# Kernel optimization log

Hardware: AMD Instinct MI355X
Metric: run time of the kernel (lower is better)

## Reference

```python
import jax, jax.numpy as jnp
import numpy as np

D_MODEL, D_STATE, D_INNER, DT_RANK, D_CONV, K = 768, 16, 1536, 48, 3, 2
B_SZ, L_SEQ = 2, 2048

def setup_inputs() -> dict:
    key = jax.random.key(0)
    ks = jax.random.split(key, 10)
    s = lambda k, shp, sc=0.02: jax.random.normal(k, shp, dtype=jnp.float32) * sc
    return {
        "x": jax.random.normal(ks[0], (B_SZ, L_SEQ, D_MODEL), dtype=jnp.float32),
        "in_proj_w": s(ks[1], (2 * D_INNER, D_MODEL)),
        "conv_w": s(ks[2], (D_INNER, 1, D_CONV), 0.3),
        "conv_b": s(ks[3], (D_INNER,), 0.1),
        "x_proj_w": s(ks[4], (K, DT_RANK + 2 * D_STATE, D_INNER)),
        "dt_proj_w": s(ks[5], (K, D_INNER, DT_RANK), 0.1),
        "dt_proj_b": s(ks[6], (K, D_INNER), 0.1),
        "A_logs": s(ks[7], (K * D_INNER, D_STATE), 0.5),
        "Ds": jnp.ones((K * D_INNER,), dtype=jnp.float32),
        "out_proj_w": s(ks[8], (D_MODEL, D_INNER)),
    }

def _selective_scan(u, delta, A, Bp, Cp, Dk):
    # u, delta: [B, L, D]; A: [D, N]; Bp, Cp: [B, L, N]; Dk: [D]
    def step(h, inp):
        d_t, u_t, b_t, c_t = inp  # [B,D], [B,D], [B,N], [B,N]
        dA = jnp.exp(d_t[..., None] * A)  # [B,D,N]
        h = h * dA + (d_t * u_t)[..., None] * b_t[:, None, :]
        y_t = jnp.einsum('bdn,bn->bd', h, c_t)
        return h, y_t
    h0 = jnp.zeros((u.shape[0], u.shape[2], A.shape[1]), dtype=u.dtype)
    xs = (jnp.swapaxes(delta, 0, 1), jnp.swapaxes(u, 0, 1),
          jnp.swapaxes(Bp, 0, 1), jnp.swapaxes(Cp, 0, 1))
    _, ys = jax.lax.scan(step, h0, xs)  # ys: [L, B, D]
    return jnp.swapaxes(ys, 0, 1) + u * Dk  # [B, L, D]

def _direction(u_k, xw_k, dtw_k, dtb_k, Alog_k, D_k):
    x_dbl = jnp.einsum('bld,rd->blr', u_k, xw_k)
    dt_in, Bp, Cp = jnp.split(x_dbl, [DT_RANK, DT_RANK + D_STATE], axis=-1)
    delta = jax.nn.softplus(jnp.einsum('blr,dr->bld', dt_in, dtw_k) + dtb_k)
    A = -jnp.exp(Alog_k)
    return _selective_scan(u_k, delta, A, Bp, Cp, D_k)

def reference(x, in_proj_w, conv_w, conv_b, x_proj_w, dt_proj_w, dt_proj_b, A_logs, Ds, out_proj_w):
    xz = x @ in_proj_w.T                       # [B, L, 2*Din]
    x_conv, z = jnp.split(xz, 2, axis=-1)
    xc = jnp.swapaxes(x_conv, 1, 2)            # [B, Din, L]
    pad = (D_CONV - 1) // 2
    xc = jax.lax.conv_general_dilated(
        xc, conv_w, window_strides=(1,), padding=[(pad, pad)],
        feature_group_count=D_INNER, dimension_numbers=('NCH', 'OIH', 'NCH'))
    xc = xc + conv_b[None, :, None]
    u = jnp.swapaxes(jax.nn.silu(xc), 1, 2)    # [B, L, Din]

    u_dirs = jnp.stack([u, jnp.flip(u, axis=1)])          # [K, B, L, Din]
    A_logs_k = A_logs.reshape(K, D_INNER, D_STATE)
    Ds_k = Ds.reshape(K, D_INNER)
    y_dirs = jax.vmap(_direction)(u_dirs, x_proj_w, dt_proj_w, dt_proj_b, A_logs_k, Ds_k)
    y_scanned = y_dirs[0] + jnp.flip(y_dirs[1], axis=1)
    y_gated = y_scanned * z
    return y_gated @ out_proj_w.T
```

## Files before the change

### kernel.cpp

```cpp
#include <hip/hip_runtime.h>
#include <math.h>

#define D_MODEL 768
#define D_STATE 16
#define D_INNER 1536
#define DT_RANK 48
#define B_SZ    2
#define L_SEQ   2048
#define CH      64
#define NCH     (L_SEQ / CH)
#define NDG     24
#define MTOT    (B_SZ * L_SEQ)
#define LOG2E   1.4426950408889634f
#define LN2     0.6931471805599453f

typedef __bf16 bf16x8 __attribute__((ext_vector_type(8)));
typedef float f32x4 __attribute__((ext_vector_type(4)));
typedef ushort ushort8_t __attribute__((ext_vector_type(8)));

__device__ __forceinline__ float ex2(float x) {
  return __builtin_amdgcn_exp2f(x);
}

__device__ __forceinline__ ushort f2bf(float f) {
  unsigned int u = __float_as_uint(f);
  unsigned int r = (u + 0x7fff + ((u >> 16) & 1)) >> 16;
  return (ushort)r;
}
__device__ __forceinline__ float bf2f(ushort u) {
  return __uint_as_float(((unsigned int)u) << 16);
}

__device__ __forceinline__ void gload_lds16(const ushort* g, ushort* l) {
  __builtin_amdgcn_global_load_lds(
      (__attribute__((address_space(1))) void*)(void*)(g),
      (__attribute__((address_space(3))) void*)(void*)(l), 16, 0, 0);
}

__device__ __forceinline__ float softplus_fast(float x) {
  return (x > 20.f) ? x : LN2 * __log2f(1.f + ex2(x * LOG2E));
}

template <int BM, int BN, int ACT, int OBF, int DTOUT>
__device__ __forceinline__ void gemm_body(
    const ushort* __restrict__ A, int lda, const ushort* __restrict__ B,
    int ldb, const float* __restrict__ bias, void* __restrict__ Cp, int ldc,
    int Nreal, int K, int bxi, int byi, ushort* __restrict__ dtin) {
  __shared__ ushort As[2][BM][32];
  __shared__ ushort Bs[2][BN][32];
  constexpr int WM = BM / 2, WN = BN / 2;
  constexpr int FM = WM / 16, FN = WN / 16;
  const int tid = threadIdx.x;
  const int lane = tid & 63;
  const int w = tid >> 6;
  const int wr = w >> 1, wc = w & 1;
  const int bm = byi * BM, bn = bxi * BN;
  const int lrow = lane >> 2;
  const int lchunk = lane & 3;
  const int fr = lane & 15;
  const int k8 = (lane >> 4) * 8;

  f32x4 acc[FM][FN] = {};

  auto stage = [&](int buf, int k0) {
    if constexpr (BM >= 64) {
#pragma unroll
      for (int g = 0; g < BM / 64; ++g) {
        const int rb = w * (BM / 4) + g * 16;
        gload_lds16(A + (size_t)(bm + rb + lrow) * lda + k0 + lchunk * 8,
                    &As[buf][rb][0]);
      }
    } else {
      if (w < 2)
        gload_lds16(A + (size_t)(bm + w * 16 + lrow) * lda + k0 + lchunk * 8,
                    &As[buf][w * 16][0]);
    }
#pragma unroll
    for (int g = 0; g < BN / 64; ++g) {
      const int rb = w * (BN / 4) + g * 16;
      gload_lds16(B + (size_t)(bn + rb + lrow) * ldb + k0 + lchunk * 8,
                  &Bs[buf][rb][0]);
    }
  };

  stage(0, 0);
  __syncthreads();
  int cur = 0;
  for (int k0 = 0; k0 < K; k0 += 32) {
    if (k0 + 32 < K) stage(cur ^ 1, k0 + 32);
    bf16x8 af[FM], bfr[FN];
#pragma unroll
    for (int m = 0; m < FM; ++m)
      af[m] =
          *reinterpret_cast<const bf16x8*>(&As[cur][wr * WM + m * 16 + fr][k8]);
#pragma unroll
    for (int n = 0; n < FN; ++n)
      bfr[n] =
          *reinterpret_cast<const bf16x8*>(&Bs[cur][wc * WN + n * 16 + fr][k8]);
#pragma unroll
    for (int m = 0; m < FM; ++m)
#pragma unroll
      for (int n = 0; n < FN; ++n)
        acc[m][n] = __builtin_amdgcn_mfma_f32_16x16x32_bf16(af[m], bfr[n],
                                                            acc[m][n], 0, 0, 0);
    __syncthreads();
    cur ^= 1;
  }

  const int row4 = (lane >> 4) * 4;
#pragma unroll
  for (int m = 0; m < FM; ++m) {
#pragma unroll
    for (int n = 0; n < FN; ++n) {
      const int gn = bn + wc * WN + n * 16 + fr;
      const int gm0 = bm + wr * WM + m * 16 + row4;
#pragma unroll
      for (int j = 0; j < 4; ++j) {
        const float v = acc[m][n][j];
        const int gm = gm0 + j;
        if (DTOUT) {
          if (gn < 64)
            dtin[(size_t)gm * 64 + gn] = (gn < 48) ? f2bf(v) : (ushort)0;
          else if (gn >= 80 && gn < 144)
            dtin[(size_t)MTOT * 64 + (size_t)gm * 64 + (gn - 80)] =
                (gn < 128) ? f2bf(v) : (ushort)0;
        }
        if (gn < Nreal) {
          float vv = v + (bias ? bias[gn] : 0.f);
          if (ACT == 1) vv = softplus_fast(vv);
          if (OBF)
            ((ushort*)Cp)[(size_t)gm * ldc + gn] = f2bf(vv);
          else
            ((float*)Cp)[(size_t)gm * ldc + gn] = vv;
        }
      }
    }
  }
}

template <int BM, int BN, int ACT, int OBF, int DTOUT>
__global__ __launch_bounds__(256) void gemm_k(
    const ushort* __restrict__ A, int lda, const ushort* __restrict__ B,
    int ldb, const float* __restrict__ bias, void* __restrict__ Cp, int ldc,
    int Nreal, int K, ushort* __restrict__ dtin) {
  gemm_body<BM, BN, ACT, OBF, DTOUT>(A, lda, B, ldb, bias, Cp, ldc, Nreal, K,
                                     blockIdx.x, blockIdx.y, dtin);
}

__global__ __launch_bounds__(256) void gemm_dt_k(
    const ushort* __restrict__ dtin, const ushort* __restrict__ w_dt,
    const float* __restrict__ dtb, ushort* __restrict__ delta) {
  const int k = blockIdx.z;
  gemm_body<64, 128, 1, 1, 0>(
      dtin + (size_t)k * MTOT * 64, 64, w_dt + (size_t)k * D_INNER * 64, 64,
      dtb + k * D_INNER, delta + (size_t)k * MTOT * D_INNER, D_INNER, D_INNER,
      64, blockIdx.x, blockIdx.y, nullptr);
}

__global__ __launch_bounds__(256) void cvt_all_kernel(
    const float* __restrict__ x, const float* __restrict__ w_in,
    const float* __restrict__ w_out, const float* __restrict__ w_xp,
    const float* __restrict__ w_dt, ushort* __restrict__ x_bf,
    ushort* __restrict__ w_in_bf, ushort* __restrict__ w_out_bf,
    ushort* __restrict__ w_xp_bf, ushort* __restrict__ w_dt_bf) {
  const long N0 = 3145728, N1 = 2359296, N2 = 1179648, N3 = 393216, N4 = 196608;
  long i = ((long)blockIdx.x * 256 + threadIdx.x) * 4;
  if (i < N0) {
    const float4 v = *(const float4*)(x + i);
    ushort4 o = {f2bf(v.x), f2bf(v.y), f2bf(v.z), f2bf(v.w)};
    *(ushort4*)(x_bf + i) = o;
    return;
  }
  i -= N0;
  if (i < N1) {
    const float4 v = *(const float4*)(w_in + i);
    ushort4 o = {f2bf(v.x), f2bf(v.y), f2bf(v.z), f2bf(v.w)};
    *(ushort4*)(w_in_bf + i) = o;
    return;
  }
  i -= N1;
  if (i < N2) {
    const float4 v = *(const float4*)(w_out + i);
    ushort4 o = {f2bf(v.x), f2bf(v.y), f2bf(v.z), f2bf(v.w)};
    *(ushort4*)(w_out_bf + i) = o;
    return;
  }
  i -= N2;
  if (i < N3) {
    const long row = i / 1536;
    ushort4 o = {0, 0, 0, 0};
    if (row < 160) {
      const float4 v = *(const float4*)(w_xp + i);
      o.x = f2bf(v.x); o.y = f2bf(v.y); o.z = f2bf(v.z); o.w = f2bf(v.w);
    }
    *(ushort4*)(w_xp_bf + i) = o;
    return;
  }
  i -= N3;
  if (i < N4) {
    const int col = (int)(i & 63);
    const long row = i >> 6;
    ushort4 o = {0, 0, 0, 0};
    if (col < 48) {
      const float4 v = *(const float4*)(w_dt + row * 48 + col);
      o.x = f2bf(v.x); o.y = f2bf(v.y); o.z = f2bf(v.z); o.w = f2bf(v.w);
    }
    *(ushort4*)(w_dt_bf + i) = o;
  }
}

__global__ __launch_bounds__(256) void conv_silu_kernel(
    const ushort* __restrict__ xz, const float* __restrict__ cw,
    const float* __restrict__ cb, ushort* __restrict__ u_bf) {
  const int nd8 = D_INNER / 8;
  const int idx = blockIdx.x * 256 + threadIdx.x;
  const int d8 = idx % nd8;
  const int lg = (idx / nd8) % (L_SEQ / 8);
  const int b = idx / (nd8 * (L_SEQ / 8));
  const int d = d8 * 8;
  const int l0 = lg * 8;

  float w0[8], w1[8], w2[8], bs[8];
#pragma unroll
  for (int j = 0; j < 8; ++j) {
    w0[j] = cw[(d + j) * 3 + 0];
    w1[j] = cw[(d + j) * 3 + 1];
    w2[j] = cw[(d + j) * 3 + 2];
    bs[j] = cb[d + j];
  }
  const ushort* base = xz + ((size_t)b * L_SEQ) * 3072 + d;
  const ushort8_t zv = {0, 0, 0, 0, 0, 0, 0, 0};
  ushort8_t prev = (l0 > 0) ? *(const ushort8_t*)(base + (size_t)(l0 - 1) * 3072) : zv;
  ushort8_t curv = *(const ushort8_t*)(base + (size_t)l0 * 3072);
#pragma unroll
  for (int i = 0; i < 8; ++i) {
    const int l = l0 + i;
    const ushort8_t nxt =
        (l + 1 < L_SEQ) ? *(const ushort8_t*)(base + (size_t)(l + 1) * 3072) : zv;
    ushort8_t o;
#pragma unroll
    for (int j = 0; j < 8; ++j) {
      const float a = bs[j] + bf2f(prev[j]) * w0[j] + bf2f(curv[j]) * w1[j] +
                      bf2f(nxt[j]) * w2[j];
      o[j] = f2bf(a / (1.f + __expf(-a)));
    }
    *(ushort8_t*)(u_bf + ((size_t)b * L_SEQ + l) * D_INNER + d) = o;
    prev = curv;
    curv = nxt;
  }
}

__global__ __launch_bounds__(128) void scan_local_kernel(
    const ushort* __restrict__ u_bf, const float* __restrict__ xdbl,
    const ushort* __restrict__ delta_bf, const float* __restrict__ A_logs,
    const float* __restrict__ Ds, ushort* __restrict__ y,
    float* __restrict__ hfin, float* __restrict__ Tsum) {
  __shared__ ushort sdu[32][64];
  __shared__ ushort suu[32][64];
  __shared__ float sB[32][16], sC[32][16];
  const int tid = threadIdx.x;
  const int lane = tid & 63;
  const int w = tid >> 6;
  const int chW = lane >> 1;
  const int half = lane & 1;
  const int bid = blockIdx.x;
  const int ch = bid & (NCH - 1);
  const int rest = bid >> 5;
  const int dgB = rest % NDG;
  const int kb = rest / NDG;
  const int b = kb & 1;
  const int k = kb >> 1;
  const int d0 = dgB * 64;
  const int dl = w * 32 + chW;
  const int d = d0 + dl;
  const int row = k * D_INNER + d;

  float An[8];
  {
    const float4 a0 =
        *(const float4*)(A_logs + (size_t)row * D_STATE + half * 8);
    const float4 a1 =
        *(const float4*)(A_logs + (size_t)row * D_STATE + half * 8 + 4);
    An[0] = -__expf(a0.x) * LOG2E; An[1] = -__expf(a0.y) * LOG2E;
    An[2] = -__expf(a0.z) * LOG2E; An[3] = -__expf(a0.w) * LOG2E;
    An[4] = -__expf(a1.x) * LOG2E; An[5] = -__expf(a1.y) * LOG2E;
    An[6] = -__expf(a1.z) * LOG2E; An[7] = -__expf(a1.w) * LOG2E;
  }
  const float Dk = Ds[row];

  const ushort* uptr = u_bf + ((size_t)b * L_SEQ) * D_INNER;
  const ushort* dptr = delta_bf + ((size_t)(k * B_SZ + b) * L_SEQ) * D_INNER;
  const float* xptr = xdbl + ((size_t)b * L_SEQ) * 160 + k * 80;
  ushort* yptr = y + ((size_t)(k * B_SZ + b) * L_SEQ) * D_INNER;

  float h[8] = {};
  float S = 0.f;

  for (int sub = 0; sub < CH / 32; ++sub) {
    const int t0 = ch * CH + sub * 32;
    const int lbase = k ? (L_SEQ - 32 - t0) : t0;
    {
      const ushort* src = (w == 0) ? dptr : uptr;
      ushort* dst = (w == 0) ? &sdu[0][0] : &suu[0][0];
#pragma unroll
      for (int i = 0; i < 4; ++i) {
        const int rd = i * 8 + (lane >> 3);
        const int gr = k ? (31 - rd) : rd;
        const int seg = lane & 7;
        gload_lds16(src + (size_t)(lbase + gr) * D_INNER + d0 + seg * 8,
                    dst + i * 512);
      }
    }
    {
      const int r = lane >> 1;
      const int ridx = k ? (31 - r) : r;
      const int c8 = (lane & 1) * 8;
      const float* srcx =
          xptr + (size_t)(lbase + r) * 160 + DT_RANK + (w ? D_STATE : 0) + c8;
      float* dstx = (w == 0) ? &sB[ridx][c8] : &sC[ridx][c8];
      *(float4*)dstx = *(const float4*)srcx;
      *(float4*)(dstx + 4) = *(const float4*)(srcx + 4);
    }
    __syncthreads();
    for (int s = 0; s < 32; ++s) {
      const float dlt = bf2f(sdu[s][dl]);
      const float uu = bf2f(suu[s][dl]);
      S += dlt;
      const float du = dlt * uu;
      const float4 Bv0 = *(const float4*)&sB[s][half * 8];
      const float4 Bv1 = *(const float4*)&sB[s][half * 8 + 4];
      const float4 Cv0 = *(const float4*)&sC[s][half * 8];
      const float4 Cv1 = *(const float4*)&sC[s][half * 8 + 4];
      h[0] = h[0] * ex2(dlt * An[0]) + du * Bv0.x;
      h[1] = h[1] * ex2(dlt * An[1]) + du * Bv0.y;
      h[2] = h[2] * ex2(dlt * An[2]) + du * Bv0.z;
      h[3] = h[3] * ex2(dlt * An[3]) + du * Bv0.w;
      h[4] = h[4] * ex2(dlt * An[4]) + du * Bv1.x;
      h[5] = h[5] * ex2(dlt * An[5]) + du * Bv1.y;
      h[6] = h[6] * ex2(dlt * An[6]) + du * Bv1.z;
      h[7] = h[7] * ex2(dlt * An[7]) + du * Bv1.w;
      float yt = h[0] * Cv0.x + h[1] * Cv0.y + h[2] * Cv0.z + h[3] * Cv0.w +
                 h[4] * Cv1.x + h[5] * Cv1.y + h[6] * Cv1.z + h[7] * Cv1.w;
      yt += __shfl_xor(yt, 1);
      if (half == 0) {
        const int t = t0 + s;
        const int l = k ? (L_SEQ - 1 - t) : t;
        yptr[(size_t)l * D_INNER + d] = f2bf(yt + uu * Dk);
      }
    }
    __syncthreads();
  }

  const size_t cidxB = ((size_t)(k * B_SZ + b) * NCH + ch) * NDG + dgB;
  *(float4*)(hfin + cidxB * 1024 + dl * 16 + half * 8) =
      make_float4(h[0], h[1], h[2], h[3]);
  *(float4*)(hfin + cidxB * 1024 + dl * 16 + half * 8 + 4) =
      make_float4(h[4], h[5], h[6], h[7]);
  if (half == 0) Tsum[cidxB * 64 + dl] = S;
}

__global__ __launch_bounds__(256) void scan_stitch_kernel(
    const float* __restrict__ hfin, const float* __restrict__ Tsum,
    const float* __restrict__ A_logs, float* __restrict__ hin) {
  const int tid = threadIdx.x;
  const int dl = tid >> 2;
  const int nq = tid & 3;
  const int bid = blockIdx.x;
  const int dgB = bid % NDG;
  const int b = (bid / NDG) & 1;
  const int k = bid / (NDG * 2);
  const int row = k * D_INNER + dgB * 64 + dl;
  const float4 alv = *(const float4*)(A_logs + (size_t)row * D_STATE + nq * 4);
  const float An0 = -__expf(alv.x) * LOG2E, An1 = -__expf(alv.y) * LOG2E;
  const float An2 = -__expf(alv.z) * LOG2E, An3 = -__expf(alv.w) * LOG2E;
  float c0 = 0.f, c1 = 0.f, c2 = 0.f, c3 = 0.f;
  for (int ch = 0; ch < NCH; ++ch) {
    const size_t cidxB = ((size_t)(k * B_SZ + b) * NCH + ch) * NDG + dgB;
    const size_t off = cidxB * 1024 + dl * 16 + nq * 4;
    *(float4*)(hin + off) = make_float4(c0, c1, c2, c3);
    const float T = Tsum[cidxB * 64 + dl];
    const float4 hf = *(const float4*)(hfin + off);
    c0 = c0 * ex2(An0 * T) + hf.x;
    c1 = c1 * ex2(An1 * T) + hf.y;
    c2 = c2 * ex2(An2 * T) + hf.z;
    c3 = c3 * ex2(An3 * T) + hf.w;
  }
}

__global__ __launch_bounds__(256) void fixup_gate_kernel(
    const float* __restrict__ xdbl, const ushort* __restrict__ delta_bf,
    const float* __restrict__ A_logs, const float* __restrict__ hin,
    const ushort* __restrict__ y, const ushort* __restrict__ xz_bf,
    ushort* __restrict__ yg) {
  __shared__ float sd0[64][64], sd1[64][64];
  __shared__ float sC0[64][16], sC1[64][16];
  __shared__ float sQF[64][4], sQB[64][4];
  const int tid = threadIdx.x;
  const int tq = tid >> 6;
  const int dl = tid & 63;
  const int bid = blockIdx.x;
  const int ch = bid & (NCH - 1);
  const int rest = bid >> 5;
  const int dgB = rest % NDG;
  const int b = rest / NDG;
  const int d0 = dgB * 64;
  const int d = d0 + dl;
  const int lbase = ch * CH;
  const int chb = NCH - 1 - ch;

  float AnF[16], AnB[16], hF[16], hB[16];
#pragma unroll
  for (int q = 0; q < 4; ++q) {
    const float4 af = *(const float4*)(A_logs + (size_t)d * D_STATE + q * 4);
    AnF[q * 4 + 0] = -__expf(af.x) * LOG2E;
    AnF[q * 4 + 1] = -__expf(af.y) * LOG2E;
    AnF[q * 4 + 2] = -__expf(af.z) * LOG2E;
    AnF[q * 4 + 3] = -__expf(af.w) * LOG2E;
    const float4 ab =
        *(const float4*)(A_logs + (size_t)(D_INNER + d) * D_STATE + q * 4);
    AnB[q * 4 + 0] = -__expf(ab.x) * LOG2E;
    AnB[q * 4 + 1] = -__expf(ab.y) * LOG2E;
    AnB[q * 4 + 2] = -__expf(ab.z) * LOG2E;
    AnB[q * 4 + 3] = -__expf(ab.w) * LOG2E;
  }
  const size_t cF = ((size_t)(0 * B_SZ + b) * NCH + ch) * NDG + dgB;
  const size_t cB = ((size_t)(1 * B_SZ + b) * NCH + chb) * NDG + dgB;
#pragma unroll
  for (int q = 0; q < 4; ++q) {
    const float4 hv = *(const float4*)(hin + cF * 1024 + dl * 16 + q * 4);
    hF[q * 4 + 0] = hv.x; hF[q * 4 + 1] = hv.y;
    hF[q * 4 + 2] = hv.z; hF[q * 4 + 3] = hv.w;
    const float4 hw = *(const float4*)(hin + cB * 1024 + dl * 16 + q * 4);
    hB[q * 4 + 0] = hw.x; hB[q * 4 + 1] = hw.y;
    hB[q * 4 + 2] = hw.z; hB[q * 4 + 3] = hw.w;
  }

  const ushort* d0p =
      delta_bf + ((size_t)(0 * B_SZ + b) * L_SEQ + lbase) * D_INNER + d0;
  const ushort* d1p =
      delta_bf + ((size_t)(1 * B_SZ + b) * L_SEQ + lbase) * D_INNER + d0;
#pragma unroll
  for (int i = 0; i < 2; ++i) {
    const int unit = tid + i * 256;
    const int r = unit >> 3, seg = unit & 7;
    const ushort8_t v0 =
        *(const ushort8_t*)(d0p + (size_t)r * D_INNER + seg * 8);
    const ushort8_t v1 =
        *(const ushort8_t*)(d1p + (size_t)r * D_INNER + seg * 8);
    *(float4*)&sd0[r][seg * 8] =
        make_float4(bf2f(v0[0]), bf2f(v0[1]), bf2f(v0[2]), bf2f(v0[3]));
    *(float4*)&sd0[r][seg * 8 + 4] =
        make_float4(bf2f(v0[4]), bf2f(v0[5]), bf2f(v0[6]), bf2f(v0[7]));
    *(float4*)&sd1[r][seg * 8] =
        make_float4(bf2f(v1[0]), bf2f(v1[1]), bf2f(v1[2]), bf2f(v1[3]));
    *(float4*)&sd1[r][seg * 8 + 4] =
        make_float4(bf2f(v1[4]), bf2f(v1[5]), bf2f(v1[6]), bf2f(v1[7]));
  }
  {
    const int r = tid >> 2;
    const int c4 = (tid & 3) * 4;
    const float* xrow = xdbl + ((size_t)b * L_SEQ + lbase + r) * 160;
    *(float4*)&sC0[r][c4] = *(const float4*)(xrow + DT_RANK + D_STATE + c4);
    *(float4*)&sC1[r][c4] =
        *(const float4*)(xrow + 80 + DT_RANK + D_STATE + c4);
  }
  __syncthreads();
  float qf = 0.f, qb = 0.f;
#pragma unroll
  for (int i = 0; i < 16; ++i) {
    qf += sd0[tq * 16 + i][dl];
    qb += sd1[tq * 16 + i][dl];
  }
  sQF[dl][tq] = qf;
  sQB[dl][tq] = qb;
  __syncthreads();
  float SF = 0.f, SB = 0.f;
#pragma unroll
  for (int j = 0; j < 4; ++j) {
    if (j < tq) SF += sQF[dl][j];
    if (j > tq) SB += sQB[dl][j];
  }

  const ushort* y0p = y + ((size_t)(0 * B_SZ + b) * L_SEQ) * D_INNER;
  const ushort* y1p = y + ((size_t)(1 * B_SZ + b) * L_SEQ) * D_INNER;
  float yacc[16];
#pragma unroll
  for (int i = 0; i < 16; ++i) {
    const int t = tq * 16 + i;
    SF += sd0[t][dl];
    float wf = 0.f;
#pragma unroll
    for (int n = 0; n < 16; ++n)
      wf += sC0[t][n] * (ex2(AnF[n] * SF) * hF[n]);
    yacc[i] = bf2f(y0p[(size_t)(lbase + t) * D_INNER + d]) + wf;
  }
#pragma unroll
  for (int i = 15; i >= 0; --i) {
    const int t = tq * 16 + i;
    SB += sd1[t][dl];
    float wb = 0.f;
#pragma unroll
    for (int n = 0; n < 16; ++n)
      wb += sC1[t][n] * (ex2(AnB[n] * SB) * hB[n]);
    yacc[i] += bf2f(y1p[(size_t)(lbase + t) * D_INNER + d]) + wb;
  }
#pragma unroll
  for (int i = 0; i < 16; ++i) {
    const int l = lbase + tq * 16 + i;
    const float z = bf2f(xz_bf[((size_t)b * L_SEQ + l) * 3072 + 1536 + d]);
    yg[((size_t)b * L_SEQ + l) * D_INNER + d] = f2bf(yacc[i] * z);
  }
}

extern "C" void kernel_launch(void* const* d_in, const int* in_sizes, int n_in,
                              void* d_out, int out_size, void* d_ws,
                              size_t ws_size, hipStream_t stream) {
  const float* x          = (const float*)d_in[0];
  const float* in_proj_w  = (const float*)d_in[1];
  const float* conv_w     = (const float*)d_in[2];
  const float* conv_b     = (const float*)d_in[3];
  const float* x_proj_w   = (const float*)d_in[4];
  const float* dt_proj_w  = (const float*)d_in[5];
  const float* dt_proj_b  = (const float*)d_in[6];
  const float* A_logs     = (const float*)d_in[7];
  const float* Ds         = (const float*)d_in[8];
  const float* out_proj_w = (const float*)d_in[9];
  float* out = (float*)d_out;

  const int M = MTOT;
  const size_t NST = (size_t)2 * B_SZ * NCH * NDG;

  float* ws    = (float*)d_ws;
  float* xdbl  = ws;
  float* hfin  = xdbl + (size_t)M * 160;
  float* hin   = hfin + NST * 1024;
  float* Tsum  = hin + NST * 1024;
  ushort* x_bf     = (ushort*)(Tsum + NST * 64);
  ushort* w_in_bf  = x_bf + (size_t)M * 768;
  ushort* w_out_bf = w_in_bf + (size_t)3072 * 768;
  ushort* w_xp_bf  = w_out_bf + (size_t)768 * 1536;
  ushort* w_dt_bf  = w_xp_bf + (size_t)256 * 1536;
  ushort* xz_bf    = w_dt_bf + (size_t)2 * 1536 * 64;
  ushort* u_bf     = xz_bf + (size_t)M * 3072;
  ushort* delta_bf = u_bf + (size_t)M * 1536;
  ushort* dtin     = delta_bf + (size_t)2 * M * 1536;
  ushort* y_bf     = dtin + (size_t)2 * M * 64;
  ushort* yg_bf    = y_bf + (size_t)2 * M * 1536;

  dim3 blk(256);
  dim3 blk128(128);

  {
    const long TOT = 3145728L + 2359296 + 1179648 + 393216 + 196608;
    cvt_all_kernel<<<dim3((TOT / 4 + 255) / 256), blk, 0, stream>>>(
        x, in_proj_w, out_proj_w, x_proj_w, dt_proj_w, x_bf, w_in_bf, w_out_bf,
        w_xp_bf, w_dt_bf);
  }

  gemm_k<128, 128, 0, 1, 0><<<dim3(3072 / 128, M / 128), blk, 0, stream>>>(
      x_bf, 768, w_in_bf, 768, nullptr, xz_bf, 3072, 3072, 768, nullptr);

  conv_silu_kernel<<<dim3(B_SZ * (L_SEQ / 8) * (D_INNER / 8) / 256), blk, 0,
                     stream>>>(xz_bf, conv_w, conv_b, u_bf);

  gemm_k<32, 64, 0, 0, 1><<<dim3(3, M / 32), blk, 0, stream>>>(
      u_bf, 1536, w_xp_bf, 1536, nullptr, xdbl, 160, 160, 1536, dtin);

  gemm_dt_k<<<dim3(1536 / 128, M / 64, 2), blk, 0, stream>>>(
      dtin, w_dt_bf, dt_proj_b, delta_bf);

  scan_local_kernel<<<dim3(2 * B_SZ * NDG * NCH), blk128, 0, stream>>>(
      u_bf, xdbl, delta_bf, A_logs, Ds, y_bf, hfin, Tsum);
  scan_stitch_kernel<<<dim3(2 * B_SZ * NDG), blk, 0, stream>>>(hfin, Tsum,
                                                               A_logs, hin);
  fixup_gate_kernel<<<dim3(B_SZ * NDG * NCH), blk, 0, stream>>>(
      xdbl, delta_bf, A_logs, hin, y_bf, xz_bf, yg_bf);

  gemm_k<128, 128, 0, 0, 0><<<dim3(768 / 128, M / 128), blk, 0, stream>>>(
      yg_bf, 1536, w_out_bf, 1536, nullptr, out, 768, 768, 1536, nullptr);
}
```

Measured before the change: 223.2 us.

## Store B/C projections as packed bf16 and give each scan thread all 16 states

The x_proj GEMM now writes the B and C columns into a compact bf16 buffer per direction and no longer writes the fp32 xdbl array. The local scan is restructured so each lane owns one channel with all 16 states, dropping the cross-lane shuffle. Each 256-thread block now has its four wavefronts handle four chunks, with B/C staged into LDS through direct global-to-LDS loads. The fixup kernel also keeps delta and C in LDS as bf16 and loads them the same way. Together this cuts global traffic and LDS footprint but raises register pressure (16 states per thread) and lowers B/C precision to bf16.

```diff
diff --git a/kernel.cpp b/kernel.cpp
--- a/kernel.cpp
+++ b/kernel.cpp
@@ -45,7 +45,8 @@
 __device__ __forceinline__ void gemm_body(
     const ushort* __restrict__ A, int lda, const ushort* __restrict__ B,
     int ldb, const float* __restrict__ bias, void* __restrict__ Cp, int ldc,
-    int Nreal, int K, int bxi, int byi, ushort* __restrict__ dtin) {
+    int Nreal, int K, int bxi, int byi, ushort* __restrict__ dtin,
+    ushort* __restrict__ bcp) {
   __shared__ ushort As[2][BM][32];
   __shared__ ushort Bs[2][BN][32];
   constexpr int WM = BM / 2, WN = BN / 2;
@@ -124,6 +125,10 @@
           else if (gn >= 80 && gn < 144)
             dtin[(size_t)MTOT * 64 + (size_t)gm * 64 + (gn - 80)] =
                 (gn < 128) ? f2bf(v) : (ushort)0;
+          if (gn >= 48 && gn < 80)
+            bcp[(size_t)gm * 32 + (gn - 48)] = f2bf(v);
+          else if (gn >= 128 && gn < 160)
+            bcp[(size_t)MTOT * 32 + (size_t)gm * 32 + (gn - 128)] = f2bf(v);
         }
         if (gn < Nreal) {
           float vv = v + (bias ? bias[gn] : 0.f);
@@ -142,9 +147,9 @@
 __global__ __launch_bounds__(256) void gemm_k(
     const ushort* __restrict__ A, int lda, const ushort* __restrict__ B,
     int ldb, const float* __restrict__ bias, void* __restrict__ Cp, int ldc,
-    int Nreal, int K, ushort* __restrict__ dtin) {
+    int Nreal, int K, ushort* __restrict__ dtin, ushort* __restrict__ bcp) {
   gemm_body<BM, BN, ACT, OBF, DTOUT>(A, lda, B, ldb, bias, Cp, ldc, Nreal, K,
-                                     blockIdx.x, blockIdx.y, dtin);
+                                     blockIdx.x, blockIdx.y, dtin, bcp);
 }
 
 __global__ __launch_bounds__(256) void gemm_dt_k(
@@ -154,7 +159,7 @@
   gemm_body<64, 128, 1, 1, 0>(
       dtin + (size_t)k * MTOT * 64, 64, w_dt + (size_t)k * D_INNER * 64, 64,
       dtb + k * D_INNER, delta + (size_t)k * MTOT * D_INNER, D_INNER, D_INNER,
-      64, blockIdx.x, blockIdx.y, nullptr);
+      64, blockIdx.x, blockIdx.y, nullptr, nullptr);
 }
 
 __global__ __launch_bounds__(256) void cvt_all_kernel(
@@ -250,113 +255,108 @@
   }
 }
 
-__global__ __launch_bounds__(128) void scan_local_kernel(
-    const ushort* __restrict__ u_bf, const float* __restrict__ xdbl,
+__global__ __launch_bounds__(256) void scan_local_kernel(
+    const ushort* __restrict__ u_bf, const ushort* __restrict__ bcb,
     const ushort* __restrict__ delta_bf, const float* __restrict__ A_logs,
     const float* __restrict__ Ds, ushort* __restrict__ y,
     float* __restrict__ hfin, float* __restrict__ Tsum) {
-  __shared__ ushort sdu[32][64];
-  __shared__ ushort suu[32][64];
-  __shared__ float sB[32][16], sC[32][16];
+  __shared__ ushort sD[4][32][64];
+  __shared__ ushort sU[4][32][64];
+  __shared__ ushort sBC[4][32][32];
   const int tid = threadIdx.x;
+  const int wid = tid >> 6;
   const int lane = tid & 63;
-  const int w = tid >> 6;
-  const int chW = lane >> 1;
-  const int half = lane & 1;
+  const int dl = lane;
   const int bid = blockIdx.x;
-  const int ch = bid & (NCH - 1);
-  const int rest = bid >> 5;
+  const int chg = bid & (NCH / 4 - 1);
+  const int rest = bid / (NCH / 4);
   const int dgB = rest % NDG;
   const int kb = rest / NDG;
   const int b = kb & 1;
   const int k = kb >> 1;
+  const int ch = chg * 4 + wid;
   const int d0 = dgB * 64;
-  const int dl = w * 32 + chW;
   const int d = d0 + dl;
   const int row = k * D_INNER + d;
 
-  float An[8];
-  {
-    const float4 a0 =
-        *(const float4*)(A_logs + (size_t)row * D_STATE + half * 8);
-    const float4 a1 =
-        *(const float4*)(A_logs + (size_t)row * D_STATE + half * 8 + 4);
-    An[0] = -__expf(a0.x) * LOG2E; An[1] = -__expf(a0.y) * LOG2E;
-    An[2] = -__expf(a0.z) * LOG2E; An[3] = -__expf(a0.w) * LOG2E;
-    An[4] = -__expf(a1.x) * LOG2E; An[5] = -__expf(a1.y) * LOG2E;
-    An[6] = -__expf(a1.z) * LOG2E; An[7] = -__expf(a1.w) * LOG2E;
+  float An[16];
+#pragma unroll
+  for (int q = 0; q < 4; ++q) {
+    const float4 a = *(const float4*)(A_logs + (size_t)row * D_STATE + q * 4);
+    An[q * 4 + 0] = -__expf(a.x) * LOG2E;
+    An[q * 4 + 1] = -__expf(a.y) * LOG2E;
+    An[q * 4 + 2] = -__expf(a.z) * LOG2E;
+    An[q * 4 + 3] = -__expf(a.w) * LOG2E;
   }
   const float Dk = Ds[row];
 
-  const ushort* uptr = u_bf + ((size_t)b * L_SEQ) * D_INNER;
-  const ushort* dptr = delta_bf + ((size_t)(k * B_SZ + b) * L_SEQ) * D_INNER;
-  const float* xptr = xdbl + ((size_t)b * L_SEQ) * 160 + k * 80;
-  ushort* yptr = y + ((size_t)(k * B_SZ + b) * L_SEQ) * D_INNER;
-
-  float h[8] = {};
+  const ushort* uptr = u_bf + (size_t)b * L_SEQ * D_INNER;
+  const ushort* dptr = delta_bf + (size_t)(k * B_SZ + b) * L_SEQ * D_INNER;
+  const ushort* bck =
+      bcb + (size_t)k * MTOT * 32 + (size_t)b * L_SEQ * 32;
+  ushort* yptr = y + (size_t)(k * B_SZ + b) * L_SEQ * D_INNER;
+
+  float h[16] = {};
   float S = 0.f;
 
   for (int sub = 0; sub < CH / 32; ++sub) {
     const int t0 = ch * CH + sub * 32;
     const int lbase = k ? (L_SEQ - 32 - t0) : t0;
     {
-      const ushort* src = (w == 0) ? dptr : uptr;
-      ushort* dst = (w == 0) ? &sdu[0][0] : &suu[0][0];
+      const int rd = lane >> 3, seg = lane & 7;
 #pragma unroll
       for (int i = 0; i < 4; ++i) {
-        const int rd = i * 8 + (lane >> 3);
-        const int gr = k ? (31 - rd) : rd;
-        const int seg = lane & 7;
-        gload_lds16(src + (size_t)(lbase + gr) * D_INNER + d0 + seg * 8,
-                    dst + i * 512);
+        const int r2 = i * 8 + rd;
+        const int gr = k ? (31 - r2) : r2;
+        const size_t off = (size_t)(lbase + gr) * D_INNER + d0 + seg * 8;
+        gload_lds16(dptr + off, &sD[wid][0][0] + i * 512);
+        gload_lds16(uptr + off, &sU[wid][0][0] + i * 512);
       }
     }
     {
-      const int r = lane >> 1;
-      const int ridx = k ? (31 - r) : r;
-      const int c8 = (lane & 1) * 8;
-      const float* srcx =
-          xptr + (size_t)(lbase + r) * 160 + DT_RANK + (w ? D_STATE : 0) + c8;
-      float* dstx = (w == 0) ? &sB[ridx][c8] : &sC[ridx][c8];
-      *(float4*)dstx = *(const float4*)srcx;
-      *(float4*)(dstx + 4) = *(const float4*)(srcx + 4);
+      const int rb = lane >> 2, sb = lane & 3;
+#pragma unroll
+      for (int i = 0; i < 2; ++i) {
+        const int r2 = i * 16 + rb;
+        const int gr = k ? (31 - r2) : r2;
+        gload_lds16(bck + (size_t)(lbase + gr) * 32 + sb * 8,
+                    &sBC[wid][0][0] + i * 512);
+      }
     }
     __syncthreads();
     for (int s = 0; s < 32; ++s) {
-      const float dlt = bf2f(sdu[s][dl]);
-      const float uu = bf2f(suu[s][dl]);
+      const float dlt = bf2f(sD[wid][s][dl]);
+      const float uu = bf2f(sU[wid][s][dl]);
       S += dlt;
       const float du = dlt * uu;
-      const float4 Bv0 = *(const float4*)&sB[s][half * 8];
-      const float4 Bv1 = *(const float4*)&sB[s][half * 8 + 4];
-      const float4 Cv0 = *(const float4*)&sC[s][half * 8];
-      const float4 Cv1 = *(const float4*)&sC[s][half * 8 + 4];
-      h[0] = h[0] * ex2(dlt * An[0]) + du * Bv0.x;
-      h[1] = h[1] * ex2(dlt * An[1]) + du * Bv0.y;
-      h[2] = h[2] * ex2(dlt * An[2]) + du * Bv0.z;
-      h[3] = h[3] * ex2(dlt * An[3]) + du * Bv0.w;
-      h[4] = h[4] * ex2(dlt * An[4]) + du * Bv1.x;
-      h[5] = h[5] * ex2(dlt * An[5]) + du * Bv1.y;
-      h[6] = h[6] * ex2(dlt * An[6]) + du * Bv1.z;
-      h[7] = h[7] * ex2(dlt * An[7]) + du * Bv1.w;
-      float yt = h[0] * Cv0.x + h[1] * Cv0.y + h[2] * Cv0.z + h[3] * Cv0.w +
-                 h[4] * Cv1.x + h[5] * Cv1.y + h[6] * Cv1.z + h[7] * Cv1.w;
-      yt += __shfl_xor(yt, 1);
-      if (half == 0) {
-        const int t = t0 + s;
-        const int l = k ? (L_SEQ - 1 - t) : t;
-        yptr[(size_t)l * D_INNER + d] = f2bf(yt + uu * Dk);
+      const ushort8_t Bv0 = *(const ushort8_t*)&sBC[wid][s][0];
+      const ushort8_t Bv1 = *(const ushort8_t*)&sBC[wid][s][8];
+      const ushort8_t Cv0 = *(const ushort8_t*)&sBC[wid][s][16];
+      const ushort8_t Cv1 = *(const ushort8_t*)&sBC[wid][s][24];
+      float yt = 0.f;
+#pragma unroll
+      for (int j = 0; j < 8; ++j) {
+        h[j] = h[j] * ex2(dlt * An[j]) + du * bf2f(Bv0[j]);
+        yt += h[j] * bf2f(Cv0[j]);
       }
+#pragma unroll
+      for (int j = 0; j < 8; ++j) {
+        h[8 + j] = h[8 + j] * ex2(dlt * An[8 + j]) + du * bf2f(Bv1[j]);
+        yt += h[8 + j] * bf2f(Cv1[j]);
+      }
+      const int t = t0 + s;
+      const int l = k ? (L_SEQ - 1 - t) : t;
+      yptr[(size_t)l * D_INNER + d] = f2bf(yt + uu * Dk);
     }
     __syncthreads();
   }
 
   const size_t cidxB = ((size_t)(k * B_SZ + b) * NCH + ch) * NDG + dgB;
-  *(float4*)(hfin + cidxB * 1024 + dl * 16 + half * 8) =
-      make_float4(h[0], h[1], h[2], h[3]);
-  *(float4*)(hfin + cidxB * 1024 + dl * 16 + half * 8 + 4) =
-      make_float4(h[4], h[5], h[6], h[7]);
-  if (half == 0) Tsum[cidxB * 64 + dl] = S;
+#pragma unroll
+  for (int q = 0; q < 4; ++q)
+    *(float4*)(hfin + cidxB * 1024 + dl * 16 + q * 4) =
+        make_float4(h[q * 4], h[q * 4 + 1], h[q * 4 + 2], h[q * 4 + 3]);
+  Tsum[cidxB * 64 + dl] = S;
 }
 
 __global__ __launch_bounds__(256) void scan_stitch_kernel(
@@ -388,16 +388,18 @@
 }
 
 __global__ __launch_bounds__(256) void fixup_gate_kernel(
-    const float* __restrict__ xdbl, const ushort* __restrict__ delta_bf,
+    const ushort* __restrict__ bcb, const ushort* __restrict__ delta_bf,
     const float* __restrict__ A_logs, const float* __restrict__ hin,
     const ushort* __restrict__ y, const ushort* __restrict__ xz_bf,
     ushort* __restrict__ yg) {
-  __shared__ float sd0[64][64], sd1[64][64];
-  __shared__ float sC0[64][16], sC1[64][16];
+  __shared__ ushort sd0[64][64], sd1[64][64];
+  __shared__ ushort sC0[64][16], sC1[64][16];
   __shared__ float sQF[64][4], sQB[64][4];
   const int tid = threadIdx.x;
-  const int tq = tid >> 6;
-  const int dl = tid & 63;
+  const int wid = tid >> 6;
+  const int lane = tid & 63;
+  const int tq = wid;
+  const int dl = lane;
   const int bid = blockIdx.x;
   const int ch = bid & (NCH - 1);
   const int rest = bid >> 5;
@@ -439,37 +441,34 @@
       delta_bf + ((size_t)(0 * B_SZ + b) * L_SEQ + lbase) * D_INNER + d0;
   const ushort* d1p =
       delta_bf + ((size_t)(1 * B_SZ + b) * L_SEQ + lbase) * D_INNER + d0;
-#pragma unroll
-  for (int i = 0; i < 2; ++i) {
-    const int unit = tid + i * 256;
-    const int r = unit >> 3, seg = unit & 7;
-    const ushort8_t v0 =
-        *(const ushort8_t*)(d0p + (size_t)r * D_INNER + seg * 8);
-    const ushort8_t v1 =
-        *(const ushort8_t*)(d1p + (size_t)r * D_INNER + seg * 8);
-    *(float4*)&sd0[r][seg * 8] =
-        make_float4(bf2f(v0[0]), bf2f(v0[1]), bf2f(v0[2]), bf2f(v0[3]));
-    *(float4*)&sd0[r][seg * 8 + 4] =
-        make_float4(bf2f(v0[4]), bf2f(v0[5]), bf2f(v0[6]), bf2f(v0[7]));
-    *(float4*)&sd1[r][seg * 8] =
-        make_float4(bf2f(v1[0]), bf2f(v1[1]), bf2f(v1[2]), bf2f(v1[3]));
-    *(float4*)&sd1[r][seg * 8 + 4] =
-        make_float4(bf2f(v1[4]), bf2f(v1[5]), bf2f(v1[6]), bf2f(v1[7]));
-  }
   {
-    const int r = tid >> 2;
-    const int c4 = (tid & 3) * 4;
-    const float* xrow = xdbl + ((size_t)b * L_SEQ + lbase + r) * 160;
-    *(float4*)&sC0[r][c4] = *(const float4*)(xrow + DT_RANK + D_STATE + c4);
-    *(float4*)&sC1[r][c4] =
-        *(const float4*)(xrow + 80 + DT_RANK + D_STATE + c4);
+    const int rd = lane >> 3, seg = lane & 7;
+#pragma unroll
+    for (int i = 0; i < 2; ++i) {
+      const int sl = i * 4 + wid;
+      const int r = sl * 8 + rd;
+      const size_t off = (size_t)r * D_INNER + seg * 8;
+      gload_lds16(d0p + off, &sd0[0][0] + sl * 512);
+      gload_lds16(d1p + off, &sd1[0][0] + sl * 512);
+    }
+  }
+  {
+    const ushort* bc0 = bcb + (size_t)b * L_SEQ * 32;
+    const ushort* bc1 = bcb + (size_t)MTOT * 32 + (size_t)b * L_SEQ * 32;
+    const int half = wid & 1;
+    const int r = half * 32 + (lane >> 1);
+    const int seg = lane & 1;
+    const ushort* src = ((wid < 2) ? bc0 : bc1) +
+                        (size_t)(lbase + r) * 32 + 16 + seg * 8;
+    ushort* dst = ((wid < 2) ? &sC0[0][0] : &sC1[0][0]) + half * 512;
+    gload_lds16(src, dst);
   }
   __syncthreads();
   float qf = 0.f, qb = 0.f;
 #pragma unroll
   for (int i = 0; i < 16; ++i) {
-    qf += sd0[tq * 16 + i][dl];
-    qb += sd1[tq * 16 + i][dl];
+    qf += bf2f(sd0[tq * 16 + i][dl]);
+    qb += bf2f(sd1[tq * 16 + i][dl]);
   }
   sQF[dl][tq] = qf;
   sQB[dl][tq] = qb;
@@ -487,21 +486,31 @@
 #pragma unroll
   for (int i = 0; i < 16; ++i) {
     const int t = tq * 16 + i;
-    SF += sd0[t][dl];
+    SF += bf2f(sd0[t][dl]);
+    const ushort8_t c0a = *(const ushort8_t*)&sC0[t][0];
+    const ushort8_t c0b = *(const ushort8_t*)&sC0[t][8];
     float wf = 0.f;
 #pragma unroll
-    for (int n = 0; n < 16; ++n)
-      wf += sC0[t][n] * (ex2(AnF[n] * SF) * hF[n]);
+    for (int n = 0; n < 8; ++n)
+      wf += bf2f(c0a[n]) * (ex2(AnF[n] * SF) * hF[n]);
+#pragma unroll
+    for (int n = 0; n < 8; ++n)
+      wf += bf2f(c0b[n]) * (ex2(AnF[8 + n] * SF) * hF[8 + n]);
     yacc[i] = bf2f(y0p[(size_t)(lbase + t) * D_INNER + d]) + wf;
   }
 #pragma unroll
   for (int i = 15; i >= 0; --i) {
     const int t = tq * 16 + i;
-    SB += sd1[t][dl];
+    SB += bf2f(sd1[t][dl]);
+    const ushort8_t c1a = *(const ushort8_t*)&sC1[t][0];
+    const ushort8_t c1b = *(const ushort8_t*)&sC1[t][8];
     float wb = 0.f;
 #pragma unroll
-    for (int n = 0; n < 16; ++n)
-      wb += sC1[t][n] * (ex2(AnB[n] * SB) * hB[n]);
+    for (int n = 0; n < 8; ++n)
+      wb += bf2f(c1a[n]) * (ex2(AnB[n] * SB) * hB[n]);
+#pragma unroll
+    for (int n = 0; n < 8; ++n)
+      wb += bf2f(c1b[n]) * (ex2(AnB[8 + n] * SB) * hB[8 + n]);
     yacc[i] += bf2f(y1p[(size_t)(lbase + t) * D_INNER + d]) + wb;
   }
 #pragma unroll
@@ -531,11 +540,11 @@
   const size_t NST = (size_t)2 * B_SZ * NCH * NDG;
 
   float* ws    = (float*)d_ws;
-  float* xdbl  = ws;
-  float* hfin  = xdbl + (size_t)M * 160;
+  float* hfin  = ws;
   float* hin   = hfin + NST * 1024;
   float* Tsum  = hin + NST * 1024;
-  ushort* x_bf     = (ushort*)(Tsum + NST * 64);
+  ushort* bcbuf    = (ushort*)(Tsum + NST * 64);
+  ushort* x_bf     = bcbuf + (size_t)2 * M * 32;
   ushort* w_in_bf  = x_bf + (size_t)M * 768;
   ushort* w_out_bf = w_in_bf + (size_t)3072 * 768;
   ushort* w_xp_bf  = w_out_bf + (size_t)768 * 1536;
@@ -548,7 +557,6 @@
   ushort* yg_bf    = y_bf + (size_t)2 * M * 1536;
 
   dim3 blk(256);
-  dim3 blk128(128);
 
   {
     const long TOT = 3145728L + 2359296 + 1179648 + 393216 + 196608;
@@ -558,24 +566,26 @@
   }
 
   gemm_k<128, 128, 0, 1, 0><<<dim3(3072 / 128, M / 128), blk, 0, stream>>>(
-      x_bf, 768, w_in_bf, 768, nullptr, xz_bf, 3072, 3072, 768, nullptr);
+      x_bf, 768, w_in_bf, 768, nullptr, xz_bf, 3072, 3072, 768, nullptr,
+      nullptr);
 
   conv_silu_kernel<<<dim3(B_SZ * (L_SEQ / 8) * (D_INNER / 8) / 256), blk, 0,
                      stream>>>(xz_bf, conv_w, conv_b, u_bf);
 
   gemm_k<32, 64, 0, 0, 1><<<dim3(3, M / 32), blk, 0, stream>>>(
-      u_bf, 1536, w_xp_bf, 1536, nullptr, xdbl, 160, 160, 1536, dtin);
+      u_bf, 1536, w_xp_bf, 1536, nullptr, nullptr, 1, 0, 1536, dtin, bcbuf);
 
   gemm_dt_k<<<dim3(1536 / 128, M / 64, 2), blk, 0, stream>>>(
       dtin, w_dt_bf, dt_proj_b, delta_bf);
 
-  scan_local_kernel<<<dim3(2 * B_SZ * NDG * NCH), blk128, 0, stream>>>(
-      u_bf, xdbl, delta_bf, A_logs, Ds, y_bf, hfin, Tsum);
+  scan_local_kernel<<<dim3(2 * B_SZ * NDG * (NCH / 4)), blk, 0, stream>>>(
+      u_bf, bcbuf, delta_bf, A_logs, Ds, y_bf, hfin, Tsum);
   scan_stitch_kernel<<<dim3(2 * B_SZ * NDG), blk, 0, stream>>>(hfin, Tsum,
                                                                A_logs, hin);
   fixup_gate_kernel<<<dim3(B_SZ * NDG * NCH), blk, 0, stream>>>(
-      xdbl, delta_bf, A_logs, hin, y_bf, xz_bf, yg_bf);
+      bcbuf, delta_bf, A_logs, hin, y_bf, xz_bf, yg_bf);
 
   gemm_k<128, 128, 0, 0, 0><<<dim3(768 / 128, M / 128), blk, 0, stream>>>(
-      yg_bf, 1536, w_out_bf, 1536, nullptr, out, 768, 768, 1536, nullptr);
-}
+      yg_bf, 1536, w_out_bf, 1536, nullptr, out, 768, 768, 1536, nullptr,
+      nullptr);
+}
```

New measurement: 239.9 us. +7.5%, slower.
